# Kernel tuning notes

Measured on AMD Instinct MI355X. Metric: run time of the kernel, lower is better.

## Reference

```python
import jax, jax.numpy as jnp
import numpy as np

B, S, M, D, H, F, E, K = 4, 1024, 1024, 1024, 16, 4096, 4, 2
DH = D // H
LB_COEF = 0.01
LN_EPS = 1e-5


def setup_inputs() -> dict:
    key = jax.random.key(0)
    ks = jax.random.split(key, 16)
    w = lambda k, shape: jax.random.normal(k, shape, jnp.float32) * 0.02
    return {
        "x": jax.random.normal(ks[0], (B, S, D), jnp.float32),
        "memory": jax.random.normal(ks[1], (B, M, D), jnp.float32),
        "sWq": w(ks[2], (D, D)), "sWk": w(ks[3], (D, D)),
        "sWv": w(ks[4], (D, D)), "sWo": w(ks[5], (D, D)),
        "cWq": w(ks[6], (D, D)), "cWk": w(ks[7], (D, D)),
        "cWv": w(ks[8], (D, D)), "cWo": w(ks[9], (D, D)),
        "Wg": w(ks[10], (E, D)),
        "W1": w(ks[11], (E, F, D)), "b1": jnp.zeros((E, F), jnp.float32),
        "W2": w(ks[12], (E, D, F)), "b2": jnp.zeros((E, D), jnp.float32),
        "ln1_g": jnp.ones((D,), jnp.float32), "ln1_b": jnp.zeros((D,), jnp.float32),
        "ln2_g": jnp.ones((D,), jnp.float32), "ln2_b": jnp.zeros((D,), jnp.float32),
        "ln3_g": jnp.ones((D,), jnp.float32), "ln3_b": jnp.zeros((D,), jnp.float32),
    }


def _ln(x, g, b):
    m = x.mean(-1, keepdims=True)
    v = ((x - m) ** 2).mean(-1, keepdims=True)
    return (x - m) * jax.lax.rsqrt(v + LN_EPS) * g + b


def _mha(q_in, k_in, v_in, Wq, Wk, Wv, Wo):
    # nn.Linear(bias=False): y = x @ W.T; split into heads [b, h, s, dh]
    def split(t):
        b, s, _ = t.shape
        return t.reshape(b, s, H, DH).transpose(0, 2, 1, 3)
    Q = split(q_in @ Wq.T)
    Kh = split(k_in @ Wk.T)
    V = split(v_in @ Wv.T)
    scores = jnp.einsum('bhqd,bhkd->bhqk', Q, Kh) / jnp.sqrt(jnp.float32(DH))
    attn = jax.nn.softmax(scores, axis=-1)  # dropout is identity in eval
    out = jnp.einsum('bhqk,bhkd->bhqd', attn, V)
    b, _, s, _ = out.shape
    out = out.transpose(0, 2, 1, 3).reshape(b, s, D)
    return out @ Wo.T


def _moe(h, Wg, W1, b1, W2, b2):
    gate_logits = h @ Wg.T                      # [B, S, E]
    gate_probs = jax.nn.softmax(gate_logits, -1)
    topk_logits, topk_idx = jax.lax.top_k(gate_logits, K)
    topk_w = jax.nn.softmax(topk_logits, -1)    # [B, S, K]
    # dense all-experts FFN (faithful to source): [B, S, E, F] hidden
    hid = jax.nn.gelu(jnp.einsum('bsd,efd->bsef', h, W1) + b1, approximate=False)
    eo = jnp.einsum('bsef,edf->bsed', hid, W2) + b2   # [B, S, E, D]
    sel = jnp.take_along_axis(eo, topk_idx[..., None], axis=2)  # [B, S, K, D]
    out = (sel * topk_w[..., None]).sum(axis=2)
    one_hot = jax.nn.one_hot(topk_idx, E, dtype=gate_probs.dtype)  # [B, S, K, E]
    load = one_hot.sum(axis=2).mean(axis=(0, 1))   # [E]
    imp = gate_probs.mean(axis=(0, 1))             # [E]
    aux = LB_COEF * (E * jnp.sum(load * imp))
    return out, aux


def reference(x, memory, sWq, sWk, sWv, sWo, cWq, cWk, cWv, cWo,
              Wg, W1, b1, W2, b2,
              ln1_g, ln1_b, ln2_g, ln2_b, ln3_g, ln3_b):
    h = _ln(x, ln1_g, ln1_b)
    x = x + _mha(h, h, h, sWq, sWk, sWv, sWo)
    h = _ln(x, ln2_g, ln2_b)
    x = x + _mha(h, memory, memory, cWq, cWk, cWv, cWo)
    h = _ln(x, ln3_g, ln3_b)
    ffn_out, aux = _moe(h, Wg, W1, b1, W2, b2)
    return (x + ffn_out, aux)
```

## Files before the change

### kernel.cpp

```cpp
#include <hip/hip_runtime.h>
#include <math.h>
#include <stdint.h>

typedef unsigned short u16;
typedef _Float16 f16;
typedef __attribute__((ext_vector_type(8))) _Float16 f16x8;
typedef __attribute__((ext_vector_type(8))) short s16x8;
typedef __attribute__((ext_vector_type(4))) float f32x4;
typedef __attribute__((ext_vector_type(4))) unsigned short u16x4;

#define DEV static __device__ __forceinline__

#define MFMA16(a, b, c) __builtin_amdgcn_mfma_f32_16x16x32_f16((a), (b), (c), 0, 0, 0)

DEV void split2(float v, u16& hi, u16& lo) {
  f16 h = (f16)v;
  f16 l = (f16)(v - (float)h);
  hi = __builtin_bit_cast(u16, h);
  lo = __builtin_bit_cast(u16, l);
}
DEV u16 f2h(float v) { f16 h = (f16)v; return __builtin_bit_cast(u16, h); }
DEV float h2f(u16 u) { f16 h = __builtin_bit_cast(f16, u); return (float)h; }

DEV void gload16(const void* gp, const void* lp) {
  typedef const __attribute__((address_space(1))) unsigned GU;
  typedef __attribute__((address_space(3))) unsigned LU;
  GU* g = (GU*)(uintptr_t)gp;
  LU* l = (LU*)(unsigned)(uintptr_t)lp;
  __builtin_amdgcn_global_load_lds(g, l, 16, 0, 0);
}

DEV int swzP(int q) { return ((q & 3) << 4) ^ (((q >> 2) & 3) << 5); }


enum { EPI3_SPLIT = 0, EPI3_RESID = 1 };

template <int EPI>
__global__ __launch_bounds__(512, 4)
void gemm3(const u16* __restrict__ Ah, const u16* __restrict__ Al,
           const u16* __restrict__ Bh, const u16* __restrict__ Bl,
           int nColT, int K, int ldC,
           u16* __restrict__ outh, u16* __restrict__ outl,
           float* __restrict__ outf, const float* __restrict__ resid)
{
  __shared__ alignas(16) u16 sAh[2][128 * 32], sAl[2][128 * 32];
  __shared__ alignas(16) u16 sBh[2][128 * 32], sBl[2][128 * 32];
  const int L = blockIdx.x;
  const int s = L >> 3;
  const int rt = (L & 7) * 4 + s / nColT;
  const int ct = s % nColT;
  const int tid = threadIdx.x;
  const int wave = tid >> 6, lane = tid & 63;
  const int wr = wave >> 2, wc = wave & 3;
  const int li = lane & 15, g = lane >> 4;
  const long row0 = (long)rt * 128;
  const int col0 = ct * 128;

  const int srow = tid >> 2;
  const int scol = ((tid & 3) ^ ((tid >> 3) & 3)) * 8;
  const long arow = (row0 + srow) * (long)K + scol;
  const long brow = ((long)col0 + srow) * (long)K + scol;
  const u16 *gAh = Ah + arow, *gAl = Al + arow;
  const u16 *gBh = Bh + brow, *gBl = Bl + brow;
  const int wbase = wave * 512;

  const f32x4 fz = {0.f, 0.f, 0.f, 0.f};
  f32x4 acc[4][2];
#pragma unroll
  for (int m = 0; m < 4; m++)
#pragma unroll
    for (int n = 0; n < 2; n++) acc[m][n] = fz;

  const int aoff = (wr * 64 + li) * 32 + (g ^ ((li >> 1) & 3)) * 8;
  const int boff = (wc * 32 + li) * 32 + (g ^ ((li >> 1) & 3)) * 8;

  gload16(gAh, &sAh[0][wbase]);
  gload16(gAl, &sAl[0][wbase]);
  gload16(gBh, &sBh[0][wbase]);
  gload16(gBl, &sBl[0][wbase]);

  int cur = 0;
  for (int k0 = 0; k0 < K; k0 += 32, cur ^= 1) {
    __syncthreads();
    const int nxt = cur ^ 1;
    if (k0 + 32 < K) {
      gload16(gAh + k0 + 32, &sAh[nxt][wbase]);
      gload16(gAl + k0 + 32, &sAl[nxt][wbase]);
      gload16(gBh + k0 + 32, &sBh[nxt][wbase]);
      gload16(gBl + k0 + 32, &sBl[nxt][wbase]);
    }
    f16x8 ah[4], al4[4], bh[2], bl4[2];
#pragma unroll
    for (int m = 0; m < 4; m++) {
      ah[m] = *(const f16x8*)(&sAh[cur][aoff + m * 512]);
      al4[m] = *(const f16x8*)(&sAl[cur][aoff + m * 512]);
    }
#pragma unroll
    for (int n = 0; n < 2; n++) {
      bh[n] = *(const f16x8*)(&sBh[cur][boff + n * 512]);
      bl4[n] = *(const f16x8*)(&sBl[cur][boff + n * 512]);
    }
#pragma unroll
    for (int m = 0; m < 4; m++)
#pragma unroll
      for (int n = 0; n < 2; n++) {
        f32x4 t = acc[m][n];
        t = MFMA16(al4[m], bh[n], t);
        t = MFMA16(ah[m], bl4[n], t);
        t = MFMA16(ah[m], bh[n], t);
        acc[m][n] = t;
      }
  }

#pragma unroll
  for (int m = 0; m < 4; m++)
#pragma unroll
    for (int n = 0; n < 2; n++) {
      const int col = col0 + wc * 32 + n * 16 + li;
#pragma unroll
      for (int r = 0; r < 4; r++) {
        const long row = row0 + wr * 64 + m * 16 + g * 4 + r;
        const long idx = row * ldC + col;
        const float v = acc[m][n][r];
        if constexpr (EPI == EPI3_SPLIT) {
          u16 hi, lo; split2(v, hi, lo);
          outh[idx] = hi; outl[idx] = lo;
        } else {
          outf[idx] = resid[idx] + v;
        }
      }
    }
}

__global__ __launch_bounds__(256)
void vtrans(const u16* __restrict__ Vh, const u16* __restrict__ Vl,
            u16* __restrict__ Th, u16* __restrict__ Tl)
{
  __shared__ u16 t0[64][80];
  __shared__ u16 t1[64][80];
  const int kb = blockIdx.x, h = blockIdx.y, b = blockIdx.z;
  const int tid = threadIdx.x;
  const int r = tid >> 2;
  const int c = tid & 3;
  const long srow = ((long)b * 1024 + kb * 64 + r) * 3072 + h * 64;
  s16x8 a0 = *(const s16x8*)(Vh + srow + c * 8);
  s16x8 a1 = *(const s16x8*)(Vh + srow + c * 8 + 32);
  s16x8 b0 = *(const s16x8*)(Vl + srow + c * 8);
  s16x8 b1 = *(const s16x8*)(Vl + srow + c * 8 + 32);
#pragma unroll
  for (int j = 0; j < 8; j++) {
    t0[c * 8 + j][r]      = (u16)(short)a0[j];
    t0[c * 8 + 32 + j][r] = (u16)(short)a1[j];
    t1[c * 8 + j][r]      = (u16)(short)b0[j];
    t1[c * 8 + 32 + j][r] = (u16)(short)b1[j];
  }
  __syncthreads();
  const int dh = tid >> 2;
  const long drow = ((long)(b * 16 + h) * 64 + dh) * 1024 + kb * 64;
  s16x8 o0, o1;
#pragma unroll
  for (int j = 0; j < 8; j++) {
    o0[j] = (short)t0[dh][c * 8 + j];
    o1[j] = (short)t0[dh][c * 8 + 32 + j];
  }
  *(s16x8*)(Th + drow + c * 8) = o0;
  *(s16x8*)(Th + drow + c * 8 + 32) = o1;
#pragma unroll
  for (int j = 0; j < 8; j++) {
    o0[j] = (short)t1[dh][c * 8 + j];
    o1[j] = (short)t1[dh][c * 8 + 32 + j];
  }
  *(s16x8*)(Tl + drow + c * 8) = o0;
  *(s16x8*)(Tl + drow + c * 8 + 32) = o1;
}

__global__ __launch_bounds__(512, 4)
void attn3(const u16* __restrict__ Qh, const u16* __restrict__ Ql,
           const u16* __restrict__ Kbh, const u16* __restrict__ Kbl,
           const u16* __restrict__ Vth, const u16* __restrict__ Vtl,
           u16* __restrict__ AOh, u16* __restrict__ AOl)
{
  __shared__ alignas(16) u16 lKh[64 * 64], lKl[64 * 64];
  __shared__ alignas(16) u16 lVh[64 * 64], lVl[64 * 64];
  __shared__ alignas(16) u16 lPh[8 * 16 * 64], lPl[8 * 16 * 64];
  const int L = blockIdx.x;
  const int idx = L >> 3;
  const int qt = idx & 7;
  const int bhp = (L & 7) * 8 + (idx >> 3);
  const int b = bhp >> 4, h = bhp & 15;
  const int tid = threadIdx.x;
  const int wave = tid >> 6, lane = tid & 63;
  const int li = lane & 15, g = lane >> 4;
  const int bh = b * 16 + h;
  const int LD = 3072;

  const long qrow0 = (long)b * 1024 + qt * 128 + wave * 16;
  f16x8 qfh[2], qfl[2];
#pragma unroll
  for (int kk = 0; kk < 2; kk++) {
    const long qoff = (qrow0 + li) * LD + h * 64 + kk * 32 + g * 8;
    qfh[kk] = *(const f16x8*)(Qh + qoff);
    qfl[kk] = *(const f16x8*)(Ql + qoff);
  }

  const f32x4 fz = {0.f, 0.f, 0.f, 0.f};
  float m_run[4], l_run[4];
  f32x4 oacc[4];
#pragma unroll
  for (int r = 0; r < 4; r++) { m_run[r] = -INFINITY; l_run[r] = 0.f; }
#pragma unroll
  for (int d = 0; d < 4; d++) oacc[d] = fz;

  char* cKh = (char*)lKh; char* cKl = (char*)lKl;
  char* cVh = (char*)lVh; char* cVl = (char*)lVl;
  char* cPh = (char*)lPh + wave * 2048;
  char* cPl = (char*)lPl + wave * 2048;

  const int kr = tid >> 3;
  const int kce = (tid & 7) * 8;
  const u16* kbase_h = Kbh + ((long)b * 1024 + kr) * LD + h * 64 + kce;
  const u16* kbase_l = Kbl + ((long)b * 1024 + kr) * LD + h * 64 + kce;
  const u16* vbase_h = Vth + ((long)bh * 64 + kr) * 1024 + kce;
  const u16* vbase_l = Vtl + ((long)bh * 64 + kr) * 1024 + kce;
  const int sdst = kr * 128 + ((kce * 2) ^ ((kr & 7) << 4));

  s16x8 rkh, rkl, rvh, rvl;
#define LOADT(t)                                                   \
  {                                                                \
    const long ko = (long)(t) * 64 * LD;                           \
    const int vo = (t) * 64;                                       \
    rkh = *(const s16x8*)(kbase_h + ko);                           \
    rkl = *(const s16x8*)(kbase_l + ko);                           \
    rvh = *(const s16x8*)(vbase_h + vo);                           \
    rvl = *(const s16x8*)(vbase_l + vo);                           \
  }

  LOADT(0);

  for (int t = 0; t < 16; ++t) {
    __syncthreads();
    *(s16x8*)(cKh + sdst) = rkh;
    *(s16x8*)(cKl + sdst) = rkl;
    *(s16x8*)(cVh + sdst) = rvh;
    *(s16x8*)(cVl + sdst) = rvl;
    if (t < 15) LOADT(t + 1);
    __syncthreads();

    f32x4 s[4];
#pragma unroll
    for (int cb = 0; cb < 4; cb++) {
      f32x4 tt = fz;
      const int key = cb * 16 + li;
#pragma unroll
      for (int kk = 0; kk < 2; kk++) {
        const int off = key * 128 + (((kk * 32 + g * 8) * 2) ^ ((key & 7) << 4));
        f16x8 fh = *(const f16x8*)(cKh + off);
        f16x8 fl = *(const f16x8*)(cKl + off);
        tt = MFMA16(qfl[kk], fh, tt);
        tt = MFMA16(qfh[kk], fl, tt);
        tt = MFMA16(qfh[kk], fh, tt);
      }
      s[cb] = tt;
    }
#pragma unroll
    for (int cb = 0; cb < 4; cb++)
#pragma unroll
      for (int r = 0; r < 4; r++) s[cb][r] *= 0.125f;

#pragma unroll
    for (int r = 0; r < 4; r++) {
      float mx = fmaxf(fmaxf(s[0][r], s[1][r]), fmaxf(s[2][r], s[3][r]));
      mx = fmaxf(mx, __shfl_xor(mx, 1));
      mx = fmaxf(mx, __shfl_xor(mx, 2));
      mx = fmaxf(mx, __shfl_xor(mx, 4));
      mx = fmaxf(mx, __shfl_xor(mx, 8));
      float mnew = fmaxf(m_run[r], mx);
      float sc = __expf(m_run[r] - mnew);
      m_run[r] = mnew;
      float ls = 0.f;
#pragma unroll
      for (int cb = 0; cb < 4; cb++) {
        float p = __expf(s[cb][r] - mnew);
        s[cb][r] = p;
        ls += p;
      }
      ls += __shfl_xor(ls, 1);
      ls += __shfl_xor(ls, 2);
      ls += __shfl_xor(ls, 4);
      ls += __shfl_xor(ls, 8);
      l_run[r] = l_run[r] * sc + ls;
#pragma unroll
      for (int d = 0; d < 4; d++) oacc[d][r] *= sc;
    }

#pragma unroll
    for (int cb = 0; cb < 4; cb++)
#pragma unroll
      for (int r = 0; r < 4; r++) {
        const int q = g * 4 + r;
        const int key = cb * 16 + li;
        const int off = q * 128 + ((key * 2) ^ swzP(q));
        u16 hi, lo; split2(s[cb][r], hi, lo);
        *(u16*)(cPh + off) = hi;
        *(u16*)(cPl + off) = lo;
      }

#pragma unroll
    for (int kk = 0; kk < 2; kk++) {
      const int kbyte = (kk * 32 + g * 8) * 2;
      const int poff = li * 128 + (kbyte ^ swzP(li));
      f16x8 pfh = *(const f16x8*)(cPh + poff);
      f16x8 pfl = *(const f16x8*)(cPl + poff);
#pragma unroll
      for (int d = 0; d < 4; d++) {
        const int dh = d * 16 + li;
        const int voff = dh * 128 + (kbyte ^ ((dh & 7) << 4));
        f16x8 vfh = *(const f16x8*)(cVh + voff);
        f16x8 vfl = *(const f16x8*)(cVl + voff);
        f32x4 tacc = oacc[d];
        tacc = MFMA16(pfl, vfh, tacc);
        tacc = MFMA16(pfh, vfl, tacc);
        tacc = MFMA16(pfh, vfh, tacc);
        oacc[d] = tacc;
      }
    }
  }
#undef LOADT

#pragma unroll
  for (int d = 0; d < 4; d++)
#pragma unroll
    for (int r = 0; r < 4; r++) {
      const long row = qrow0 + g * 4 + r;
      const int col = h * 64 + d * 16 + li;
      u16 hi, lo; split2(oacc[d][r] / l_run[r], hi, lo);
      AOh[row * 1024 + col] = hi;
      AOl[row * 1024 + col] = lo;
    }
}

template <bool GATE>
__global__ __launch_bounds__(256)
void ln_kernel(const float* __restrict__ x, const float* __restrict__ gam,
               const float* __restrict__ bet, u16* __restrict__ hh,
               u16* __restrict__ hl,
               const float* __restrict__ Wg, float* __restrict__ glog)
{
  const int row = blockIdx.x;
  const int tid = threadIdx.x;
  const int wave = tid >> 6, lane = tid & 63;
  const float* xr = x + (long)row * 1024;
  float4 v = *(const float4*)(xr + tid * 4);
  float s = v.x + v.y + v.z + v.w;
  float s2 = v.x * v.x + v.y * v.y + v.z * v.z + v.w * v.w;
#pragma unroll
  for (int m = 1; m < 64; m <<= 1) { s += __shfl_xor(s, m); s2 += __shfl_xor(s2, m); }
  __shared__ float red1[4], red2[4];
  if (lane == 0) { red1[wave] = s; red2[wave] = s2; }
  __syncthreads();
  float S = red1[0] + red1[1] + red1[2] + red1[3];
  float S2 = red2[0] + red2[1] + red2[2] + red2[3];
  float mean = S * (1.f / 1024.f);
  float var = S2 * (1.f / 1024.f) - mean * mean;
  float rstd = 1.f / sqrtf(var + 1e-5f);
  const int c = tid * 4;
  float hv[4];
  hv[0] = (v.x - mean) * rstd * gam[c + 0] + bet[c + 0];
  hv[1] = (v.y - mean) * rstd * gam[c + 1] + bet[c + 1];
  hv[2] = (v.z - mean) * rstd * gam[c + 2] + bet[c + 2];
  hv[3] = (v.w - mean) * rstd * gam[c + 3] + bet[c + 3];
  u16x4 oh, ol;
#pragma unroll
  for (int j = 0; j < 4; j++) {
    u16 hi, lo; split2(hv[j], hi, lo);
    oh[j] = hi; ol[j] = lo;
  }
  *(u16x4*)(hh + (long)row * 1024 + c) = oh;
  *(u16x4*)(hl + (long)row * 1024 + c) = ol;

  if constexpr (GATE) {
    float pe[4];
#pragma unroll
    for (int e = 0; e < 4; e++) {
      const float* wr_ = Wg + e * 1024 + c;
      pe[e] = hv[0] * wr_[0] + hv[1] * wr_[1] + hv[2] * wr_[2] + hv[3] * wr_[3];
    }
#pragma unroll
    for (int e = 0; e < 4; e++)
#pragma unroll
      for (int m = 1; m < 64; m <<= 1) pe[e] += __shfl_xor(pe[e], m);
    __shared__ float gred[4][4];
    if (lane == 0) {
#pragma unroll
      for (int e = 0; e < 4; e++) gred[wave][e] = pe[e];
    }
    __syncthreads();
    if (tid < 4)
      glog[(long)row * 4 + tid] = gred[0][tid] + gred[1][tid] + gred[2][tid] + gred[3][tid];
  }
}

__global__ __launch_bounds__(256)
void route_kernel(const float* __restrict__ glog,
                  int* __restrict__ tlist, float* __restrict__ wrow,
                  int4* __restrict__ meta, float2* __restrict__ wts,
                  int* __restrict__ scanMeta, float* __restrict__ outAux)
{
  const int tid = threadIdx.x;
  const int lane = tid & 63, wave = tid >> 6;
  __shared__ int scn[4][256];
  __shared__ int sTot[4];
  __shared__ int sBase[4];
  __shared__ float sred[4][8];

  for (int r = tid; r < 8704; r += 256) { tlist[r] = 0; wrow[r] = 0.f; }

  int myCnt[4] = {0, 0, 0, 0};
  float imp[4] = {0.f, 0.f, 0.f, 0.f}, ld[4] = {0.f, 0.f, 0.f, 0.f};
  unsigned char e1s[16], e2s[16];
  float w1s[16], w2s[16];
#pragma unroll 1
  for (int j = 0; j < 16; j++) {
    const int t = tid * 16 + j;
    float l[4];
#pragma unroll
    for (int e = 0; e < 4; e++) l[e] = glog[t * 4 + e];
    int e1 = 0; float bv = l[0];
#pragma unroll
    for (int e = 1; e < 4; e++) if (l[e] > bv) { bv = l[e]; e1 = e; }
    int e2 = -1; float bv2 = -INFINITY;
#pragma unroll
    for (int e = 0; e < 4; e++) if (e != e1 && l[e] > bv2) { bv2 = l[e]; e2 = e; }
    float wq = expf(bv2 - bv);
    float w1 = 1.f / (1.f + wq), w2 = wq / (1.f + wq);
    float ps = 0.f, pv[4];
#pragma unroll
    for (int e = 0; e < 4; e++) { pv[e] = expf(l[e] - bv); ps += pv[e]; }
    float inv = 1.f / ps;
#pragma unroll
    for (int e = 0; e < 4; e++) imp[e] += pv[e] * inv;
    ld[e1] += 1.f; ld[e2] += 1.f;
    myCnt[e1]++; myCnt[e2]++;
    e1s[j] = (unsigned char)e1; e2s[j] = (unsigned char)e2;
    w1s[j] = w1; w2s[j] = w2;
  }
#pragma unroll
  for (int e = 0; e < 4; e++) scn[e][tid] = myCnt[e];
  __syncthreads();

  if (wave < 4) {
    int carry = 0;
    for (int seg = 0; seg < 4; seg++) {
      int v = scn[wave][seg * 64 + lane];
      const int orig = v;
#pragma unroll
      for (int d = 1; d < 64; d <<= 1) { int o = __shfl_up(v, d); if (lane >= d) v += o; }
      scn[wave][seg * 64 + lane] = carry + v - orig;
      carry += __shfl(v, 63);
    }
    if (lane == 0) sTot[wave] = carry;
  }
  __syncthreads();

  if (tid == 0) {
    int base = 0;
    for (int e = 0; e < 4; e++) {
      const int c = sTot[e];
      const int cap = (c + 127) & ~127;
      sBase[e] = base;
      const int t0 = base >> 7, t1 = (base + cap) >> 7;
      for (int i = t0; i < t1; i++) scanMeta[1 + i] = e;
      base += cap;
    }
    scanMeta[0] = base >> 7;
  }
  __syncthreads();

  int off[4];
#pragma unroll
  for (int e = 0; e < 4; e++) off[e] = sBase[e] + scn[e][tid];
#pragma unroll 1
  for (int j = 0; j < 16; j++) {
    const int t = tid * 16 + j;
    const int e1 = e1s[j], e2 = e2s[j];
    const int p1 = off[e1]++;
    const int p2 = off[e2]++;
    tlist[p1] = t; wrow[p1] = w1s[j];
    tlist[p2] = t; wrow[p2] = w2s[j];
    int4 m; m.x = p1; m.y = p2; m.z = e1; m.w = e2;
    meta[t] = m;
    float2 w; w.x = w1s[j]; w.y = w2s[j];
    wts[t] = w;
  }

#pragma unroll
  for (int e = 0; e < 4; e++) {
#pragma unroll
    for (int d = 1; d < 64; d <<= 1) {
      imp[e] += __shfl_xor(imp[e], d);
      ld[e] += __shfl_xor(ld[e], d);
    }
  }
  if (lane == 0) {
#pragma unroll
    for (int e = 0; e < 4; e++) { sred[wave][e] = imp[e]; sred[wave][4 + e] = ld[e]; }
  }
  __syncthreads();
  if (tid == 0) {
    float a = 0.f;
    for (int e = 0; e < 4; e++) {
      float im = sred[0][e] + sred[1][e] + sred[2][e] + sred[3][e];
      float lo = sred[0][4 + e] + sred[1][4 + e] + sred[2][4 + e] + sred[3][4 + e];
      a += (lo * (1.f / 4096.f)) * (im * (1.f / 4096.f));
    }
    outAux[0] = 0.01f * 4.f * a;
  }
}

__global__ __launch_bounds__(256, 2)
void gemm_up(const u16* __restrict__ A, const u16* __restrict__ w1h,
             const float* __restrict__ b1, const int* __restrict__ tlist,
             const float* __restrict__ wrow, const int* __restrict__ scanMeta,
             u16* __restrict__ hid)
{
  const int L = blockIdx.x;
  const int gg = (L & 7) * 272 + (L >> 3);
  const int rt = gg >> 5, cc = gg & 31;
  if (rt >= scanMeta[0]) return;
  const int e = scanMeta[1 + rt];
  __shared__ alignas(16) u16 lA[2][128 * 32];
  __shared__ alignas(16) u16 lB[2][128 * 32];
  const int tid = threadIdx.x;
  const int wave = tid >> 6, lane = tid & 63;
  const int wr = wave >> 1, wc = wave & 1;
  const int li = lane & 15, g = lane >> 4;
  const int row0 = rt * 128;
  const int col0 = cc * 128;

  const int srow = lane >> 2;
  const int scol = ((lane & 3) ^ ((lane >> 3) & 3)) * 8;
  const int r1 = row0 + wave * 32 + srow;
  const long t1 = tlist[r1], t2 = tlist[r1 + 16];
  const u16* gA1 = A + t1 * 1024 + scol;
  const u16* gA2 = A + t2 * 1024 + scol;
  const u16* gB = w1h + (size_t)e * 4194304 +
                  ((size_t)(col0 + wave * 32 + srow)) * 1024 + scol;
  const int wbase = wave * 1024;

  const f32x4 fz = {0.f, 0.f, 0.f, 0.f};
  f32x4 acc[4][4];
#pragma unroll
  for (int m = 0; m < 4; m++)
#pragma unroll
    for (int n = 0; n < 4; n++) acc[m][n] = fz;

  const int aoff = (wr * 64 + li) * 32 + (g ^ ((li >> 1) & 3)) * 8;
  const int boff = (wc * 64 + li) * 32 + (g ^ ((li >> 1) & 3)) * 8;

  gload16(gA1, &lA[0][wbase]);
  gload16(gA2, &lA[0][wbase + 512]);
  gload16(gB, &lB[0][wbase]);
  gload16(gB + 16 * 1024, &lB[0][wbase + 512]);

  int cur = 0;
  for (int k0 = 0; k0 < 1024; k0 += 32, cur ^= 1) {
    __syncthreads();
    const int nxt = cur ^ 1;
    if (k0 + 32 < 1024) {
      gload16(gA1 + k0 + 32, &lA[nxt][wbase]);
      gload16(gA2 + k0 + 32, &lA[nxt][wbase + 512]);
      gload16(gB + k0 + 32, &lB[nxt][wbase]);
      gload16(gB + k0 + 32 + 16 * 1024, &lB[nxt][wbase + 512]);
    }
    f16x8 af[4], bfr[4];
#pragma unroll
    for (int m = 0; m < 4; m++) af[m] = *(const f16x8*)(&lA[cur][aoff + m * 512]);
#pragma unroll
    for (int n = 0; n < 4; n++) bfr[n] = *(const f16x8*)(&lB[cur][boff + n * 512]);
#pragma unroll
    for (int m = 0; m < 4; m++)
#pragma unroll
      for (int n = 0; n < 4; n++)
        acc[m][n] = MFMA16(af[m], bfr[n], acc[m][n]);
  }

#pragma unroll
  for (int m = 0; m < 4; m++)
#pragma unroll
    for (int n = 0; n < 4; n++) {
      const int col = col0 + wc * 64 + n * 16 + li;
#pragma unroll
      for (int r = 0; r < 4; r++) {
        const int row = row0 + wr * 64 + m * 16 + g * 4 + r;
        const float coef = wrow[row];
        float tv = acc[m][n][r] + b1[e * 4096 + col];
        float z = 1.59576912f * tv * (1.f + 0.044715f * tv * tv);
        float ge = tv / (1.f + __expf(-z));
        hid[(size_t)row * 4096 + col] = f2h(coef * ge);
      }
    }
}

__global__ __launch_bounds__(512, 4)
void gemm_down(const u16* __restrict__ hid, const u16* __restrict__ w2h,
               const int* __restrict__ scanMeta, u16* __restrict__ part)
{
  const int L = blockIdx.x;
  const int gg = (L & 7) * 68 + (L >> 3);
  const int rt = gg >> 3, cc = gg & 7;
  if (rt >= scanMeta[0]) return;
  const int e = scanMeta[1 + rt];
  __shared__ alignas(16) u16 lA[2][128 * 32];
  __shared__ alignas(16) u16 lB[2][128 * 32];
  const int tid = threadIdx.x;
  const int wave = tid >> 6, lane = tid & 63;
  const int wr = wave >> 2, wc = wave & 3;
  const int li = lane & 15, g = lane >> 4;
  const int row0 = rt * 128;
  const int col0 = cc * 128;

  const int srow = tid >> 2;
  const int scol = ((tid & 3) ^ ((tid >> 3) & 3)) * 8;
  const u16* gA = hid + ((size_t)(row0 + srow)) * 4096 + scol;
  const u16* gB = w2h + (size_t)e * 4194304 +
                  ((size_t)(col0 + srow)) * 4096 + scol;
  const int wbase = wave * 512;

  const f32x4 fz = {0.f, 0.f, 0.f, 0.f};
  f32x4 acc[4][2];
#pragma unroll
  for (int m = 0; m < 4; m++)
#pragma unroll
    for (int n = 0; n < 2; n++) acc[m][n] = fz;

  const int aoff = (wr * 64 + li) * 32 + (g ^ ((li >> 1) & 3)) * 8;
  const int boff = (wc * 32 + li) * 32 + (g ^ ((li >> 1) & 3)) * 8;

  gload16(gA, &lA[0][wbase]);
  gload16(gB, &lB[0][wbase]);

  int cur = 0;
  for (int k0 = 0; k0 < 4096; k0 += 32, cur ^= 1) {
    __syncthreads();
    const int nxt = cur ^ 1;
    if (k0 + 32 < 4096) {
      gload16(gA + k0 + 32, &lA[nxt][wbase]);
      gload16(gB + k0 + 32, &lB[nxt][wbase]);
    }
    f16x8 af[4], bfr[2];
#pragma unroll
    for (int m = 0; m < 4; m++) af[m] = *(const f16x8*)(&lA[cur][aoff + m * 512]);
#pragma unroll
    for (int n = 0; n < 2; n++) bfr[n] = *(const f16x8*)(&lB[cur][boff + n * 512]);
#pragma unroll
    for (int m = 0; m < 4; m++)
#pragma unroll
      for (int n = 0; n < 2; n++)
        acc[m][n] = MFMA16(af[m], bfr[n], acc[m][n]);
  }

#pragma unroll
  for (int m = 0; m < 4; m++)
#pragma unroll
    for (int n = 0; n < 2; n++) {
      const int col = col0 + wc * 32 + n * 16 + li;
#pragma unroll
      for (int r = 0; r < 4; r++) {
        const int row = row0 + wr * 64 + m * 16 + g * 4 + r;
        part[(size_t)row * 1024 + col] = f2h(acc[m][n][r]);
      }
    }
}

__global__ __launch_bounds__(256)
void merge_kernel(const float* __restrict__ xw, const u16* __restrict__ part,
                  const int4* __restrict__ meta, const float2* __restrict__ wts,
                  const float* __restrict__ b2, float* __restrict__ out)
{
  const long i = ((long)blockIdx.x * 256 + threadIdx.x) * 4;
  const int row = (int)(i >> 10), col = (int)(i & 1023);
  const int4 m = meta[row];
  const float2 w = wts[row];
  float4 a = *(const float4*)(xw + i);
  u16x4 p1 = *(const u16x4*)(part + (size_t)m.x * 1024 + col);
  u16x4 p2 = *(const u16x4*)(part + (size_t)m.y * 1024 + col);
  const float* b2a = b2 + m.z * 1024 + col;
  const float* b2b = b2 + m.w * 1024 + col;
  float av[4] = {a.x, a.y, a.z, a.w};
  float4 o;
  float ov[4];
#pragma unroll
  for (int j = 0; j < 4; j++)
    ov[j] = av[j] + h2f(p1[j]) + h2f(p2[j]) + w.x * b2a[j] + w.y * b2b[j];
  o.x = ov[0]; o.y = ov[1]; o.z = ov[2]; o.w = ov[3];
  *(float4*)(out + i) = o;
}

__global__ __launch_bounds__(256)
void cvt_h(const float* __restrict__ src, u16* __restrict__ dst)
{
  const long i = ((long)blockIdx.x * 256 + threadIdx.x) * 4;
  float4 v = *(const float4*)(src + i);
  u16x4 o = {f2h(v.x), f2h(v.y), f2h(v.z), f2h(v.w)};
  *(u16x4*)(dst + i) = o;
}

__global__ __launch_bounds__(256)
void cvt_split(const float* __restrict__ src, u16* __restrict__ dh, u16* __restrict__ dl)
{
  const long i = ((long)blockIdx.x * 256 + threadIdx.x) * 4;
  float4 v = *(const float4*)(src + i);
  u16x4 oh, ol;
  float vv[4] = {v.x, v.y, v.z, v.w};
#pragma unroll
  for (int j = 0; j < 4; j++) { u16 a, b; split2(vv[j], a, b); oh[j] = a; ol[j] = b; }
  *(u16x4*)(dh + i) = oh;
  *(u16x4*)(dl + i) = ol;
}

struct Ptr8 { const float* p[8]; };

__global__ __launch_bounds__(256)
void cvt8_split(Ptr8 ps, u16* __restrict__ dh, u16* __restrict__ dl)
{
  const int w = blockIdx.y;
  const long i = ((long)blockIdx.x * 256 + threadIdx.x) * 4;
  float4 v = *(const float4*)(ps.p[w] + i);
  u16x4 oh, ol;
  float vv[4] = {v.x, v.y, v.z, v.w};
#pragma unroll
  for (int j = 0; j < 4; j++) { u16 a, b; split2(vv[j], a, b); oh[j] = a; ol[j] = b; }
  *(u16x4*)(dh + (long)w * 1048576 + i) = oh;
  *(u16x4*)(dl + (long)w * 1048576 + i) = ol;
}

extern "C" void kernel_launch(void* const* d_in, const int* in_sizes, int n_in,
                              void* d_out, int out_size, void* d_ws, size_t ws_size,
                              hipStream_t stream)
{
  const float* x    = (const float*)d_in[0];
  const float* mem  = (const float*)d_in[1];
  const float* sWq  = (const float*)d_in[2];
  const float* sWk  = (const float*)d_in[3];
  const float* sWv  = (const float*)d_in[4];
  const float* sWo  = (const float*)d_in[5];
  const float* cWq  = (const float*)d_in[6];
  const float* cWk  = (const float*)d_in[7];
  const float* cWv  = (const float*)d_in[8];
  const float* cWo  = (const float*)d_in[9];
  const float* Wg   = (const float*)d_in[10];
  const float* W1   = (const float*)d_in[11];
  const float* b1   = (const float*)d_in[12];
  const float* W2   = (const float*)d_in[13];
  const float* b2   = (const float*)d_in[14];
  const float* ln1g = (const float*)d_in[15];
  const float* ln1b = (const float*)d_in[16];
  const float* ln2g = (const float*)d_in[17];
  const float* ln2b = (const float*)d_in[18];
  const float* ln3g = (const float*)d_in[19];
  const float* ln3b = (const float*)d_in[20];
  float* out = (float*)d_out;
  (void)in_sizes; (void)n_in; (void)out_size; (void)ws_size;

  char* ws = (char*)d_ws;
  size_t off = 0;
  auto alloc = [&](size_t bytes) -> void* {
    void* p = ws + off; off += (bytes + 255) & ~(size_t)255; return p;
  };
  float* xw    = (float*)alloc((size_t)4096 * 1024 * 4);
  u16*   hh    = (u16*)  alloc((size_t)4096 * 1024 * 2);
  u16*   hl    = (u16*)  alloc((size_t)4096 * 1024 * 2);
  u16*   memh  = (u16*)  alloc((size_t)4096 * 1024 * 2);
  u16*   meml  = (u16*)  alloc((size_t)4096 * 1024 * 2);
  u16*   qkvh  = (u16*)  alloc((size_t)4096 * 3072 * 2);
  u16*   qkvl  = (u16*)  alloc((size_t)4096 * 3072 * 2);
  u16*   aoh   = (u16*)  alloc((size_t)4096 * 1024 * 2);
  u16*   aol   = (u16*)  alloc((size_t)4096 * 1024 * 2);
  u16*   aWh   = (u16*)  alloc((size_t)8 * 1024 * 1024 * 2);
  u16*   aWl   = (u16*)  alloc((size_t)8 * 1024 * 1024 * 2);
  u16*   w1h   = (u16*)  alloc((size_t)4 * 4096 * 1024 * 2);
  u16*   w2h   = (u16*)  alloc((size_t)4 * 4096 * 1024 * 2);
  float* glog  = (float*)alloc((size_t)4096 * 4 * 4);
  int*   tlist = (int*)  alloc((size_t)8704 * 4);
  float* wrow  = (float*)alloc((size_t)8704 * 4);
  int4*  meta  = (int4*) alloc((size_t)4096 * 16);
  float2* wts  = (float2*)alloc((size_t)4096 * 8);
  int*   scanM = (int*)  alloc((size_t)128 * 4);
  u16*   vth = hh;
  u16*   vtl = hl;
  u16*   hid = qkvh;
  u16*   part = (u16*)hh;

  Ptr8 p8;
  p8.p[0] = sWq; p8.p[1] = sWk; p8.p[2] = sWv; p8.p[3] = sWo;
  p8.p[4] = cWq; p8.p[5] = cWk; p8.p[6] = cWv; p8.p[7] = cWo;
  cvt8_split<<<dim3(1024, 8), 256, 0, stream>>>(p8, aWh, aWl);
  cvt_h<<<16384, 256, 0, stream>>>(W1, w1h);
  cvt_h<<<16384, 256, 0, stream>>>(W2, w2h);
  cvt_split<<<4096, 256, 0, stream>>>(mem, memh, meml);

  ln_kernel<false><<<4096, 256, 0, stream>>>(x, ln1g, ln1b, hh, hl, nullptr, nullptr);
  gemm3<EPI3_SPLIT><<<768, 512, 0, stream>>>(hh, hl, aWh, aWl, 24, 1024, 3072,
                                             qkvh, qkvl, nullptr, nullptr);
  vtrans<<<dim3(16, 16, 4), 256, 0, stream>>>(qkvh + 2048, qkvl + 2048, vth, vtl);
  attn3<<<512, 512, 0, stream>>>(qkvh, qkvl, qkvh + 1024, qkvl + 1024,
                                 vth, vtl, aoh, aol);
  gemm3<EPI3_RESID><<<256, 512, 0, stream>>>(aoh, aol, aWh + (size_t)3 * 1048576,
                                             aWl + (size_t)3 * 1048576, 8, 1024, 1024,
                                             nullptr, nullptr, xw, x);

  ln_kernel<false><<<4096, 256, 0, stream>>>(xw, ln2g, ln2b, hh, hl, nullptr, nullptr);
  gemm3<EPI3_SPLIT><<<256, 512, 0, stream>>>(hh, hl, aWh + (size_t)4 * 1048576,
                                             aWl + (size_t)4 * 1048576, 8, 1024, 3072,
                                             qkvh, qkvl, nullptr, nullptr);
  gemm3<EPI3_SPLIT><<<512, 512, 0, stream>>>(memh, meml, aWh + (size_t)5 * 1048576,
                                             aWl + (size_t)5 * 1048576, 16, 1024, 3072,
                                             qkvh + 1024, qkvl + 1024, nullptr, nullptr);
  vtrans<<<dim3(16, 16, 4), 256, 0, stream>>>(qkvh + 2048, qkvl + 2048, vth, vtl);
  attn3<<<512, 512, 0, stream>>>(qkvh, qkvl, qkvh + 1024, qkvl + 1024,
                                 vth, vtl, aoh, aol);
  gemm3<EPI3_RESID><<<256, 512, 0, stream>>>(aoh, aol, aWh + (size_t)7 * 1048576,
                                             aWl + (size_t)7 * 1048576, 8, 1024, 1024,
                                             nullptr, nullptr, xw, xw);

  ln_kernel<true><<<4096, 256, 0, stream>>>(xw, ln3g, ln3b, hh, hl, Wg, glog);
  route_kernel<<<1, 256, 0, stream>>>(glog, tlist, wrow, meta, wts, scanM,
                                      out + (size_t)4096 * 1024);
  gemm_up<<<2176, 256, 0, stream>>>(hh, w1h, b1, tlist, wrow, scanM, hid);
  gemm_down<<<544, 512, 0, stream>>>(hid, w2h, scanM, part);
  merge_kernel<<<4096, 256, 0, stream>>>(xw, part, meta, wts, b2, out);
}
```

Measured before the change: 745.9 us.

## Compute softmax row sums via MFMA and remap MoE GEMM tile schedules

In the flash-attention kernel, the per-row probability sum is no longer built from scalar adds and cross-lane shuffles. It is now accumulated with two extra MFMAs against a ones vector, one on the hi half and one on the lo half of P, which removes the shuffle reductions. The gemm_up launch bound is raised to 4 blocks per CU, and both MoE GEMMs get a new block-to-tile mapping that changes how row and column tiles are spread across XCDs, aiming for better weight reuse in L2. The row sum now comes from the f16-split P values rather than the fp32 values, and the higher occupancy target may force register spills in gemm_up.

Result: slower. 765.3 us (+2.6%).

```diff
diff --git a/kernel.cpp b/kernel.cpp
--- a/kernel.cpp
+++ b/kernel.cpp
@@ -204,10 +204,14 @@
   }
 
   const f32x4 fz = {0.f, 0.f, 0.f, 0.f};
-  float m_run[4], l_run[4];
+  f16x8 one8;
+#pragma unroll
+  for (int j = 0; j < 8; j++) one8[j] = (f16)1.f;
+  float m_run[4];
+  f32x4 lsum = fz;
   f32x4 oacc[4];
 #pragma unroll
-  for (int r = 0; r < 4; r++) { m_run[r] = -INFINITY; l_run[r] = 0.f; }
+  for (int r = 0; r < 4; r++) m_run[r] = -INFINITY;
 #pragma unroll
   for (int d = 0; d < 4; d++) oacc[d] = fz;
 
@@ -277,18 +281,9 @@
       float mnew = fmaxf(m_run[r], mx);
       float sc = __expf(m_run[r] - mnew);
       m_run[r] = mnew;
-      float ls = 0.f;
-#pragma unroll
-      for (int cb = 0; cb < 4; cb++) {
-        float p = __expf(s[cb][r] - mnew);
-        s[cb][r] = p;
-        ls += p;
-      }
-      ls += __shfl_xor(ls, 1);
-      ls += __shfl_xor(ls, 2);
-      ls += __shfl_xor(ls, 4);
-      ls += __shfl_xor(ls, 8);
-      l_run[r] = l_run[r] * sc + ls;
+#pragma unroll
+      for (int cb = 0; cb < 4; cb++) s[cb][r] = __expf(s[cb][r] - mnew);
+      lsum[r] *= sc;
 #pragma unroll
       for (int d = 0; d < 4; d++) oacc[d][r] *= sc;
     }
@@ -323,6 +318,8 @@
         tacc = MFMA16(pfh, vfh, tacc);
         oacc[d] = tacc;
       }
+      lsum = MFMA16(pfh, one8, lsum);
+      lsum = MFMA16(pfl, one8, lsum);
     }
   }
 #undef LOADT
@@ -333,7 +330,7 @@
     for (int r = 0; r < 4; r++) {
       const long row = qrow0 + g * 4 + r;
       const int col = h * 64 + d * 16 + li;
-      u16 hi, lo; split2(oacc[d][r] / l_run[r], hi, lo);
+      u16 hi, lo; split2(oacc[d][r] / lsum[r], hi, lo);
       AOh[row * 1024 + col] = hi;
       AOl[row * 1024 + col] = lo;
     }
@@ -517,15 +514,16 @@
   }
 }
 
-__global__ __launch_bounds__(256, 2)
+__global__ __launch_bounds__(256, 4)
 void gemm_up(const u16* __restrict__ A, const u16* __restrict__ w1h,
              const float* __restrict__ b1, const int* __restrict__ tlist,
              const float* __restrict__ wrow, const int* __restrict__ scanMeta,
              u16* __restrict__ hid)
 {
   const int L = blockIdx.x;
-  const int gg = (L & 7) * 272 + (L >> 3);
-  const int rt = gg >> 5, cc = gg & 31;
+  const int s = L >> 3;
+  const int cc = (L & 7) * 4 + s / 68;
+  const int rt = s % 68;
   if (rt >= scanMeta[0]) return;
   const int e = scanMeta[1 + rt];
   __shared__ alignas(16) u16 lA[2][128 * 32];
@@ -606,8 +604,8 @@
                const int* __restrict__ scanMeta, u16* __restrict__ part)
 {
   const int L = blockIdx.x;
-  const int gg = (L & 7) * 68 + (L >> 3);
-  const int rt = gg >> 3, cc = gg & 7;
+  const int cc = L & 7;
+  const int rt = L >> 3;
   if (rt >= scanMeta[0]) return;
   const int e = scanMeta[1 + rt];
   __shared__ alignas(16) u16 lA[2][128 * 32];
```
